# Optimization experiments

Hardware: AMD Instinct MI355X
Metric: run time of the kernel (lower is better)

The kernel has to match this reference:

```python
import jax, jax.numpy as jnp
import numpy as np

N = 50000
HEADS = 3
NEG_SLOPE = 0.2


def _add_self_loops(edge_index, num_nodes):
    loops = jnp.arange(num_nodes, dtype=edge_index.dtype)
    return jnp.concatenate([edge_index, jnp.stack([loops, loops])], axis=1)


def _gcn_conv(x, edge_index, W, b):
    # PyG GCNConv: add self loops, symmetric deg^-1/2 normalization.
    ei = _add_self_loops(edge_index, x.shape[0])
    src, dst = ei[0], ei[1]
    deg = jax.ops.segment_sum(jnp.ones_like(dst, dtype=x.dtype), dst, num_segments=x.shape[0])
    dinv = jax.lax.rsqrt(deg)  # deg >= 1 due to self loops
    norm = dinv[src] * dinv[dst]                      # [E']
    xw = x @ W                                        # [N, F_out]
    out = jax.ops.segment_sum(xw[src] * norm[:, None], dst, num_segments=x.shape[0])
    return out + b


def _gat_conv(x, edge_index, W, att_src, att_dst, b):
    # PyG GATConv (concat=True): self loops, per-edge attention, segment softmax.
    n = x.shape[0]
    ei = _add_self_loops(edge_index, n)
    src, dst = ei[0], ei[1]
    h = (x @ W).reshape(n, HEADS, -1)                 # [N, H, C]
    a_s = (h * att_src).sum(-1)                       # [N, H]
    a_d = (h * att_dst).sum(-1)                       # [N, H]
    e = jax.nn.leaky_relu(a_s[src] + a_d[dst], NEG_SLOPE)   # [E', H]
    m = jax.ops.segment_max(e, dst, num_segments=n)   # [N, H] per-dst max
    e = jnp.exp(e - m[dst])
    s = jax.ops.segment_sum(e, dst, num_segments=n)   # [N, H]
    alpha = e / s[dst]                                # [E', H]
    out = jax.ops.segment_sum(h[src] * alpha[:, :, None], dst, num_segments=n)
    return out.reshape(n, -1) + b                     # [N, H*C]


def setup_inputs() -> dict:
    key = jax.random.key(0)
    ks = jax.random.split(key, 9)
    in_ch, out_ch = 256, 64
    hid = 2 * out_ch  # 128
    E = 800000
    x = jax.random.normal(ks[0], (N, in_ch), dtype=jnp.float32)
    edge_index = jax.random.randint(ks[1], (2, E), 0, N, dtype=jnp.int32)
    W1 = jax.random.normal(ks[2], (in_ch, hid), dtype=jnp.float32) / np.sqrt(in_ch)
    b1 = jnp.zeros((hid,), dtype=jnp.float32)
    W2 = jax.random.normal(ks[3], (hid, HEADS * out_ch), dtype=jnp.float32) / np.sqrt(hid)
    att_src = jax.random.normal(ks[4], (HEADS, out_ch), dtype=jnp.float32) / np.sqrt(out_ch)
    att_dst = jax.random.normal(ks[5], (HEADS, out_ch), dtype=jnp.float32) / np.sqrt(out_ch)
    b2 = jnp.zeros((HEADS * out_ch,), dtype=jnp.float32)
    return {"x": x, "edge_index": edge_index, "W1": W1, "b1": b1,
            "W2": W2, "att_src": att_src, "att_dst": att_dst, "b2": b2}


def reference(x, edge_index, W1, b1, W2, att_src, att_dst, b2):
    h = jax.nn.relu(_gcn_conv(x, edge_index, W1, b1))
    # F.dropout(training=False) is identity in eval mode
    h = _gat_conv(h, edge_index, W2, att_src, att_dst, b2)
    return jax.nn.relu(h)
```

## Files before the change

kernel.cpp:

```cpp
#include <hip/hip_runtime.h>
#include <hip/hip_fp16.h>
#include <math.h>

#define NODES    50000
#define IN_CH    256
#define HID      128
#define HEADS    3
#define HC       64
#define OC       (HEADS*HC)
#define NEG_SLOPE 0.2f

typedef _Float16 half8_t __attribute__((ext_vector_type(8)));
typedef _Float16 half4_t __attribute__((ext_vector_type(4)));
typedef float float4_t __attribute__((ext_vector_type(4)));

__device__ __forceinline__ float lrelu(float v) { return v > 0.f ? v : NEG_SLOPE * v; }

__device__ __forceinline__ unsigned fkey(float f) {
    unsigned b = __float_as_uint(f);
    return (b & 0x80000000u) ? ~b : (b | 0x80000000u);
}
__device__ __forceinline__ float fdec(unsigned k) {
    unsigned b = (k & 0x80000000u) ? (k ^ 0x80000000u) : ~k;
    return __uint_as_float(b);
}

__global__ __launch_bounds__(256) void k_hist(const int* __restrict__ dst, int E, int* __restrict__ cnt,
                                              unsigned short* __restrict__ rank,
                                              const float* __restrict__ W1, const float* __restrict__ W2,
                                              _Float16* __restrict__ W1t, _Float16* __restrict__ W2t) {
    int e = blockIdx.x * 256 + threadIdx.x;
    if (e < E) {
        int r = atomicAdd(&cnt[dst[e]], 1);
        rank[e] = (unsigned short)r;
    }
    if (e < IN_CH * HID) {
        int c = e >> 8, k = e & 255;
        W1t[e] = (_Float16)W1[(size_t)k * HID + c];
    } else if (e < IN_CH * HID + HID * OC) {
        int u = e - IN_CH * HID;
        int c = u >> 7, k = u & 127;
        W2t[u] = (_Float16)W2[(size_t)k * OC + c];
    }
}

__global__ __launch_bounds__(1024) void k_scanA(const int* __restrict__ cnt, int* __restrict__ off,
                                                float* __restrict__ dinv, int* __restrict__ bsum, int n) {
    __shared__ int wsums[16];
    int tid = threadIdx.x, lane = tid & 63, wid = tid >> 6;
    int i = blockIdx.x * 1024 + tid;
    int v = (i < n) ? cnt[i] : 0;
    int incl = v;
    #pragma unroll
    for (int d = 1; d < 64; d <<= 1) {
        int t = __shfl_up(incl, d, 64);
        if (lane >= d) incl += t;
    }
    if (lane == 63) wsums[wid] = incl;
    __syncthreads();
    if (tid == 0) {
        int run = 0;
        #pragma unroll
        for (int j = 0; j < 16; j++) { int t = wsums[j]; wsums[j] = run; run += t; }
        bsum[blockIdx.x] = run;
    }
    __syncthreads();
    if (i < n) {
        off[i] = wsums[wid] + incl - v;
        dinv[i] = rsqrtf((float)(v + 1));
    }
}

__global__ __launch_bounds__(64) void k_scanB(const int* __restrict__ bsum, int* __restrict__ bbase,
                                              int* __restrict__ off, int nb, int n) {
    int tid = threadIdx.x;
    int v = (tid < nb) ? bsum[tid] : 0;
    int incl = v;
    #pragma unroll
    for (int d = 1; d < 64; d <<= 1) {
        int t = __shfl_up(incl, d, 64);
        if (tid >= d) incl += t;
    }
    bbase[tid] = incl - v;
    if (tid == 63) off[n] = incl;
}

__global__ __launch_bounds__(256) void k_scanC(int* __restrict__ off, const int* __restrict__ bbase, int n) {
    int i = blockIdx.x * 256 + threadIdx.x;
    if (i < n) off[i] += bbase[i >> 10];
}

__global__ __launch_bounds__(256) void k_fillg1(const int* __restrict__ src, const int* __restrict__ dst, int E,
                                                const int* __restrict__ off, const unsigned short* __restrict__ rank,
                                                unsigned short* __restrict__ csr,
                                                const float* __restrict__ x, const _Float16* __restrict__ W1t,
                                                const float* __restrict__ dinv, _Float16* __restrict__ xwh,
                                                int n, int fillBlocks) {
    if ((int)blockIdx.x < fillBlocks) {
        int e = blockIdx.x * 256 + threadIdx.x;
        if (e < E) {
            int d = dst[e];
            int p = off[d] + (int)rank[e];
            csr[p] = (unsigned short)src[e];
        }
        return;
    }

    int bid = blockIdx.x - fillBlocks;
    int wid = threadIdx.x >> 6, lane = threadIdx.x & 63;
    int lrow = lane & 15, kgrp = lane >> 4;
    int arow = bid * 64 + wid * 16 + lrow;
    bool rv = arow < n;
    const float* xp = x + (size_t)arow * IN_CH + kgrp * 8;

    float4_t acc[8];
    #pragma unroll
    for (int s = 0; s < 8; s++) acc[s] = (float4_t)(0.f);

    #pragma unroll
    for (int kc = 0; kc < IN_CH; kc += 32) {
        float4 a0, a1;
        if (rv) { a0 = *(const float4*)(xp + kc); a1 = *(const float4*)(xp + kc + 4); }
        else { a0 = make_float4(0.f,0.f,0.f,0.f); a1 = a0; }
        half8_t af;
        af[0]=(_Float16)a0.x; af[1]=(_Float16)a0.y; af[2]=(_Float16)a0.z; af[3]=(_Float16)a0.w;
        af[4]=(_Float16)a1.x; af[5]=(_Float16)a1.y; af[6]=(_Float16)a1.z; af[7]=(_Float16)a1.w;
        #pragma unroll
        for (int s = 0; s < 8; s++) {
            const _Float16* bp = W1t + (size_t)(s * 16 + lrow) * IN_CH + kc + kgrp * 8;
            half8_t bf = *(const half8_t*)bp;
            acc[s] = __builtin_amdgcn_mfma_f32_16x16x32_f16(af, bf, acc[s], 0, 0, 0);
        }
    }

    int orow0 = bid * 64 + wid * 16 + kgrp * 4;
    #pragma unroll
    for (int r = 0; r < 4; r++) {
        int orow = orow0 + r;
        if (orow < n) {
            float sc = dinv[orow];
            _Float16* po = xwh + ((size_t)orow << 7) + lrow;
            #pragma unroll
            for (int s = 0; s < 8; s++) po[s * 16] = (_Float16)(sc * acc[s][r]);
        }
    }
}

__global__ __launch_bounds__(256) void k_gcn(const _Float16* __restrict__ xwh, const unsigned short* __restrict__ csr,
                                             const int* __restrict__ off, const float* __restrict__ dinv,
                                             const float* __restrict__ b1, _Float16* __restrict__ hh, int n) {
    int w = (blockIdx.x * 256 + threadIdx.x) >> 6;
    int lane = threadIdx.x & 63;
    if (w >= n) return;
    int egrp = lane >> 4;
    int c8 = (lane & 15) * 8;
    float acc[8];
    #pragma unroll
    for (int j = 0; j < 8; j++) acc[j] = 0.f;

    int beg = off[w], end = off[w + 1];
    int i = beg;
    for (; i + 16 <= end; i += 16) {
        int s0 = csr[i + egrp];
        int s1 = csr[i + 4 + egrp];
        int s2 = csr[i + 8 + egrp];
        int s3 = csr[i + 12 + egrp];
        half8_t v0 = *(const half8_t*)(xwh + ((size_t)s0 << 7) + c8);
        half8_t v1 = *(const half8_t*)(xwh + ((size_t)s1 << 7) + c8);
        half8_t v2 = *(const half8_t*)(xwh + ((size_t)s2 << 7) + c8);
        half8_t v3 = *(const half8_t*)(xwh + ((size_t)s3 << 7) + c8);
        half8_t p01 = v0 + v1;
        half8_t p23 = v2 + v3;
        #pragma unroll
        for (int j = 0; j < 8; j++)
            acc[j] += (float)p01[j] + (float)p23[j];
    }
    for (; i + 4 <= end; i += 4) {
        int s = csr[i + egrp];
        half8_t v = *(const half8_t*)(xwh + ((size_t)s << 7) + c8);
        #pragma unroll
        for (int j = 0; j < 8; j++) acc[j] += (float)v[j];
    }
    if (i < end && egrp < (end - i)) {
        int s = csr[i + egrp];
        half8_t v = *(const half8_t*)(xwh + ((size_t)s << 7) + c8);
        #pragma unroll
        for (int j = 0; j < 8; j++) acc[j] += (float)v[j];
    }

    #pragma unroll
    for (int j = 0; j < 8; j++) {
        acc[j] += __shfl_xor(acc[j], 16, 64);
        acc[j] += __shfl_xor(acc[j], 32, 64);
    }
    if (egrp == 0) {
        float di = dinv[w];
        half8_t self = *(const half8_t*)(xwh + ((size_t)w << 7) + c8);
        float4 bb0 = *(const float4*)(b1 + c8);
        float4 bb1 = *(const float4*)(b1 + c8 + 4);
        float bv[8] = {bb0.x, bb0.y, bb0.z, bb0.w, bb1.x, bb1.y, bb1.z, bb1.w};
        half8_t o;
        #pragma unroll
        for (int j = 0; j < 8; j++)
            o[j] = (_Float16)fmaxf(fmaf(di, acc[j] + (float)self[j], bv[j]), 0.f);
        *(half8_t*)(hh + ((size_t)w << 7) + c8) = o;
    }
}

__global__ __launch_bounds__(256) void k_gemm2m(const _Float16* __restrict__ hh, const _Float16* __restrict__ W2t,
                                                _Float16* __restrict__ h2h, int n) {
    int wid = threadIdx.x >> 6, lane = threadIdx.x & 63;
    int lrow = lane & 15, kgrp = lane >> 4;
    int arow = blockIdx.x * 64 + wid * 16 + lrow;
    bool rv = arow < n;
    const _Float16* hp = hh + ((size_t)arow << 7) + kgrp * 8;

    float4_t acc[12];
    #pragma unroll
    for (int s = 0; s < 12; s++) acc[s] = (float4_t)(0.f);

    #pragma unroll
    for (int kc = 0; kc < HID; kc += 32) {
        half8_t af = (half8_t)((_Float16)0.f);
        if (rv) af = *(const half8_t*)(hp + kc);
        #pragma unroll
        for (int s = 0; s < 12; s++) {
            const _Float16* bp = W2t + (size_t)(s * 16 + lrow) * HID + kc + kgrp * 8;
            half8_t bf = *(const half8_t*)bp;
            acc[s] = __builtin_amdgcn_mfma_f32_16x16x32_f16(af, bf, acc[s], 0, 0, 0);
        }
    }

    int orow0 = blockIdx.x * 64 + wid * 16 + kgrp * 4;
    #pragma unroll
    for (int r = 0; r < 4; r++) {
        int orow = orow0 + r;
        if (orow < n) {
            _Float16* po = h2h + ((size_t)orow << 8) + lrow;
            #pragma unroll
            for (int s = 0; s < 12; s++) po[s * 16] = (_Float16)acc[s][r];
        }
    }
}

__global__ __launch_bounds__(256) void k_att(const _Float16* __restrict__ h2h, const float* __restrict__ att_s,
                                             const float* __restrict__ att_d, float* __restrict__ a_s4,
                                             float* __restrict__ a_d4, int n) {
    int w = (blockIdx.x * 256 + threadIdx.x) >> 6;
    int lane = threadIdx.x & 63;
    if (w >= n) return;
    bool act = lane < 48;
    int ll = act ? lane : (lane - 48);
    int hd = ll >> 4;
    int c4 = ll * 4;

    half4_t hv = *(const half4_t*)(h2h + ((size_t)w << 8) + c4);
    float4 as = *(const float4*)(att_s + c4);
    float4 ad = *(const float4*)(att_d + c4);
    float vs = (float)hv[0] * as.x + (float)hv[1] * as.y + (float)hv[2] * as.z + (float)hv[3] * as.w;
    float vd = (float)hv[0] * ad.x + (float)hv[1] * ad.y + (float)hv[2] * ad.z + (float)hv[3] * ad.w;
    #pragma unroll
    for (int o = 1; o < 16; o <<= 1) {
        vs += __shfl_xor(vs, o, 64);
        vd += __shfl_xor(vd, o, 64);
    }
    if (act && (ll & 15) == 0) {
        a_s4[w * 4 + hd] = vs;
        a_d4[w * 4 + hd] = vd;
    }
}

__global__ __launch_bounds__(1024) void k_asmax(const float* __restrict__ a_s4, int n, unsigned* __restrict__ asmaxk) {
    int i = blockIdx.x * 1024 + threadIdx.x;
    float m0 = -1e30f, m1 = -1e30f, m2 = -1e30f;
    if (i < n) {
        float4 v = *(const float4*)(a_s4 + (size_t)i * 4);
        m0 = v.x; m1 = v.y; m2 = v.z;
    }
    #pragma unroll
    for (int o = 32; o > 0; o >>= 1) {
        m0 = fmaxf(m0, __shfl_xor(m0, o, 64));
        m1 = fmaxf(m1, __shfl_xor(m1, o, 64));
        m2 = fmaxf(m2, __shfl_xor(m2, o, 64));
    }
    __shared__ float sm[16][3];
    int lane = threadIdx.x & 63, wid = threadIdx.x >> 6;
    if (lane == 0) { sm[wid][0] = m0; sm[wid][1] = m1; sm[wid][2] = m2; }
    __syncthreads();
    if (threadIdx.x == 0) {
        for (int j = 1; j < 16; j++) {
            m0 = fmaxf(m0, sm[j][0]); m1 = fmaxf(m1, sm[j][1]); m2 = fmaxf(m2, sm[j][2]);
        }
        atomicMax(asmaxk + 0, fkey(m0));
        atomicMax(asmaxk + 1, fkey(m1));
        atomicMax(asmaxk + 2, fkey(m2));
    }
}

#define GAT_EDGE(ev, hv) do { \
    float wl = __expf(lrelu((ev) + adh) - Ch); \
    ssum += wl; \
    a0 = fmaf(wl, (float)(hv)[0], a0); \
    a1 = fmaf(wl, (float)(hv)[1], a1); \
    a2 = fmaf(wl, (float)(hv)[2], a2); \
    a3 = fmaf(wl, (float)(hv)[3], a3); \
} while (0)

__global__ __launch_bounds__(256) void k_gat(const _Float16* __restrict__ h2h, const unsigned short* __restrict__ csr,
                                             const int* __restrict__ off, const float* __restrict__ a_s4,
                                             const float* __restrict__ a_d4, const unsigned* __restrict__ asmaxk,
                                             const float* __restrict__ b2, float* __restrict__ out, int n) {
    int w = (blockIdx.x * 256 + threadIdx.x) >> 6;
    int lane = threadIdx.x & 63;
    if (w >= n) return;
    bool act = lane < 48;
    int ll = act ? lane : (lane - 48);
    int hd = ll >> 4;
    int c4 = ll * 4;

    float adh = a_d4[w * 4 + hd];
    float Ch  = lrelu(fdec(asmaxk[hd]) + adh);
    float ash = a_s4[w * 4 + hd];
    float wsl = __expf(lrelu(ash + adh) - Ch);
    float ssum = wsl;
    half4_t hv = *(const half4_t*)(h2h + ((size_t)w << 8) + c4);
    float a0 = wsl * (float)hv[0], a1 = wsl * (float)hv[1];
    float a2 = wsl * (float)hv[2], a3 = wsl * (float)hv[3];

    int beg = off[w], end = off[w + 1];
    int i = beg;
    for (; i + 4 <= end; i += 4) {
        int sA = csr[i], sB = csr[i + 1], sC = csr[i + 2], sD = csr[i + 3];
        float eA = a_s4[(size_t)sA * 4 + hd];
        float eB = a_s4[(size_t)sB * 4 + hd];
        float eC = a_s4[(size_t)sC * 4 + hd];
        float eD = a_s4[(size_t)sD * 4 + hd];
        half4_t hA = *(const half4_t*)(h2h + ((size_t)sA << 8) + c4);
        half4_t hB = *(const half4_t*)(h2h + ((size_t)sB << 8) + c4);
        half4_t hC = *(const half4_t*)(h2h + ((size_t)sC << 8) + c4);
        half4_t hD = *(const half4_t*)(h2h + ((size_t)sD << 8) + c4);
        GAT_EDGE(eA, hA); GAT_EDGE(eB, hB); GAT_EDGE(eC, hC); GAT_EDGE(eD, hD);
    }
    for (; i < end; i++) {
        int s = csr[i];
        float ev = a_s4[(size_t)s * 4 + hd];
        half4_t hx = *(const half4_t*)(h2h + ((size_t)s << 8) + c4);
        GAT_EDGE(ev, hx);
    }

    if (act) {
        float inv = 1.f / ssum;
        float4 bb = *(const float4*)(b2 + c4);
        float4 o;
        o.x = fmaxf(fmaf(a0, inv, bb.x), 0.f);
        o.y = fmaxf(fmaf(a1, inv, bb.y), 0.f);
        o.z = fmaxf(fmaf(a2, inv, bb.z), 0.f);
        o.w = fmaxf(fmaf(a3, inv, bb.w), 0.f);
        *(float4*)(out + (size_t)w * OC + c4) = o;
    }
}

extern "C" void kernel_launch(void* const* d_in, const int* in_sizes, int n_in,
                              void* d_out, int out_size, void* d_ws, size_t ws_size,
                              hipStream_t stream) {
    const float* x        = (const float*)d_in[0];
    const int*   ei       = (const int*)d_in[1];
    const float* W1       = (const float*)d_in[2];
    const float* b1       = (const float*)d_in[3];
    const float* W2       = (const float*)d_in[4];
    const float* att_src  = (const float*)d_in[5];
    const float* att_dst  = (const float*)d_in[6];
    const float* b2       = (const float*)d_in[7];
    float* out = (float*)d_out;

    const int n = in_sizes[0] / IN_CH;
    const int E = in_sizes[1] / 2;
    const int* src = ei;
    const int* dst = ei + E;

    char* ws = (char*)d_ws;
    int*            cnt    = (int*)(ws + 0);
    unsigned*       asmaxk = (unsigned*)(ws + 200704);
    int*            off    = (int*)(ws + 200960);
    float*          dinv   = (float*)(ws + 401664);
    int*            bsum   = (int*)(ws + 602368);
    int*            bbase  = (int*)(ws + 602624);
    _Float16*       W1t    = (_Float16*)(ws + 602880);
    _Float16*       W2t    = (_Float16*)(ws + 668416);
    unsigned short* csr    = (unsigned short*)(ws + 717568);
    unsigned short* rank   = (unsigned short*)(ws + 2317568);
    float*          a_s4   = (float*)(ws + 3917568);
    float*          a_d4   = (float*)(ws + 4717568);
    _Float16*       xwh    = (_Float16*)(ws + 5517568);
    _Float16*       hh     = (_Float16*)(ws + 18317568);
    _Float16*       h2h    = (_Float16*)(ws + 31117568);

    (void)hipMemsetAsync(ws, 0, 200720, stream);

    int egrid = (E + 255) / 256;
    int nb = (n + 1023) / 1024;
    int gm = (n + 63) / 64;
    k_hist<<<egrid, 256, 0, stream>>>(dst, E, cnt, rank, W1, W2, W1t, W2t);
    k_scanA<<<nb, 1024, 0, stream>>>(cnt, off, dinv, bsum, n);
    k_scanB<<<1, 64, 0, stream>>>(bsum, bbase, off, nb, n);
    k_scanC<<<(n + 255) / 256, 256, 0, stream>>>(off, bbase, n);

    k_fillg1<<<egrid + gm, 256, 0, stream>>>(src, dst, E, off, rank, csr,
                                             x, W1t, dinv, xwh, n, egrid);

    int ngrid = (n + 3) / 4;
    k_gcn<<<ngrid, 256, 0, stream>>>(xwh, csr, off, dinv, b1, hh, n);

    k_gemm2m<<<gm, 256, 0, stream>>>(hh, W2t, h2h, n);

    k_att<<<ngrid, 256, 0, stream>>>(h2h, att_src, att_dst, a_s4, a_d4, n);
    k_asmax<<<nb, 1024, 0, stream>>>(a_s4, n, asmaxk);
    k_gat<<<ngrid, 256, 0, stream>>>(h2h, csr, off, a_s4, a_d4, asmaxk, b2, out, n);
}
```

Baseline: 224.3 us.

## Fuse attention-score computation into second GEMM and compact h2 row stride

Merges the separate attention-coefficient kernel into the second GEMM: each block stages its output tile in shared memory and computes per-head a_s/a_d dot products from there, so h2 is not re-read from global memory and one launch is removed. The h2 row stride also shrinks from 256 to 192 halves, which cuts the buffer footprint and makes the gathers in the GAT kernel denser. The cost is extra shared memory, a block barrier, and a serial 16-row loop per wave in the GEMM kernel.

```diff
diff --git a/kernel.cpp b/kernel.cpp
--- a/kernel.cpp
+++ b/kernel.cpp
@@ -207,8 +207,11 @@
     }
 }
 
-__global__ __launch_bounds__(256) void k_gemm2m(const _Float16* __restrict__ hh, const _Float16* __restrict__ W2t,
-                                                _Float16* __restrict__ h2h, int n) {
+__global__ __launch_bounds__(256) void k_gemm2att(const _Float16* __restrict__ hh, const _Float16* __restrict__ W2t,
+                                                  const float* __restrict__ att_s, const float* __restrict__ att_d,
+                                                  _Float16* __restrict__ h2h, float* __restrict__ a_s4,
+                                                  float* __restrict__ a_d4, int n) {
+    __shared__ _Float16 hs2[64][200];
     int wid = threadIdx.x >> 6, lane = threadIdx.x & 63;
     int lrow = lane & 15, kgrp = lane >> 4;
     int arow = blockIdx.x * 64 + wid * 16 + lrow;
@@ -235,38 +238,43 @@
     #pragma unroll
     for (int r = 0; r < 4; r++) {
         int orow = orow0 + r;
+        int rloc = wid * 16 + kgrp * 4 + r;
         if (orow < n) {
-            _Float16* po = h2h + ((size_t)orow << 8) + lrow;
+            _Float16* po = h2h + (size_t)orow * OC + lrow;
             #pragma unroll
-            for (int s = 0; s < 12; s++) po[s * 16] = (_Float16)acc[s][r];
-        }
-    }
-}
-
-__global__ __launch_bounds__(256) void k_att(const _Float16* __restrict__ h2h, const float* __restrict__ att_s,
-                                             const float* __restrict__ att_d, float* __restrict__ a_s4,
-                                             float* __restrict__ a_d4, int n) {
-    int w = (blockIdx.x * 256 + threadIdx.x) >> 6;
-    int lane = threadIdx.x & 63;
-    if (w >= n) return;
+            for (int s = 0; s < 12; s++) {
+                _Float16 hv = (_Float16)acc[s][r];
+                po[s * 16] = hv;
+                hs2[rloc][s * 16 + lrow] = hv;
+            }
+        } else {
+            #pragma unroll
+            for (int s = 0; s < 12; s++) hs2[rloc][s * 16 + lrow] = (_Float16)0.f;
+        }
+    }
+    __syncthreads();
+
     bool act = lane < 48;
     int ll = act ? lane : (lane - 48);
     int hd = ll >> 4;
     int c4 = ll * 4;
-
-    half4_t hv = *(const half4_t*)(h2h + ((size_t)w << 8) + c4);
     float4 as = *(const float4*)(att_s + c4);
     float4 ad = *(const float4*)(att_d + c4);
-    float vs = (float)hv[0] * as.x + (float)hv[1] * as.y + (float)hv[2] * as.z + (float)hv[3] * as.w;
-    float vd = (float)hv[0] * ad.x + (float)hv[1] * ad.y + (float)hv[2] * ad.z + (float)hv[3] * ad.w;
-    #pragma unroll
-    for (int o = 1; o < 16; o <<= 1) {
-        vs += __shfl_xor(vs, o, 64);
-        vd += __shfl_xor(vd, o, 64);
-    }
-    if (act && (ll & 15) == 0) {
-        a_s4[w * 4 + hd] = vs;
-        a_d4[w * 4 + hd] = vd;
+    for (int j = 0; j < 16; j++) {
+        int rloc = wid * 16 + j;
+        int orow = blockIdx.x * 64 + rloc;
+        half4_t hv = *(const half4_t*)&hs2[rloc][c4];
+        float vs = (float)hv[0] * as.x + (float)hv[1] * as.y + (float)hv[2] * as.z + (float)hv[3] * as.w;
+        float vd = (float)hv[0] * ad.x + (float)hv[1] * ad.y + (float)hv[2] * ad.z + (float)hv[3] * ad.w;
+        #pragma unroll
+        for (int o = 1; o < 16; o <<= 1) {
+            vs += __shfl_xor(vs, o, 64);
+            vd += __shfl_xor(vd, o, 64);
+        }
+        if (act && (ll & 15) == 0 && orow < n) {
+            a_s4[orow * 4 + hd] = vs;
+            a_d4[orow * 4 + hd] = vd;
+        }
     }
 }
 
@@ -323,7 +331,7 @@
     float ash = a_s4[w * 4 + hd];
     float wsl = __expf(lrelu(ash + adh) - Ch);
     float ssum = wsl;
-    half4_t hv = *(const half4_t*)(h2h + ((size_t)w << 8) + c4);
+    half4_t hv = *(const half4_t*)(h2h + (size_t)w * OC + c4);
     float a0 = wsl * (float)hv[0], a1 = wsl * (float)hv[1];
     float a2 = wsl * (float)hv[2], a3 = wsl * (float)hv[3];
 
@@ -335,16 +343,16 @@
         float eB = a_s4[(size_t)sB * 4 + hd];
         float eC = a_s4[(size_t)sC * 4 + hd];
         float eD = a_s4[(size_t)sD * 4 + hd];
-        half4_t hA = *(const half4_t*)(h2h + ((size_t)sA << 8) + c4);
-        half4_t hB = *(const half4_t*)(h2h + ((size_t)sB << 8) + c4);
-        half4_t hC = *(const half4_t*)(h2h + ((size_t)sC << 8) + c4);
-        half4_t hD = *(const half4_t*)(h2h + ((size_t)sD << 8) + c4);
+        half4_t hA = *(const half4_t*)(h2h + (size_t)sA * OC + c4);
+        half4_t hB = *(const half4_t*)(h2h + (size_t)sB * OC + c4);
+        half4_t hC = *(const half4_t*)(h2h + (size_t)sC * OC + c4);
+        half4_t hD = *(const half4_t*)(h2h + (size_t)sD * OC + c4);
         GAT_EDGE(eA, hA); GAT_EDGE(eB, hB); GAT_EDGE(eC, hC); GAT_EDGE(eD, hD);
     }
     for (; i < end; i++) {
         int s = csr[i];
         float ev = a_s4[(size_t)s * 4 + hd];
-        half4_t hx = *(const half4_t*)(h2h + ((size_t)s << 8) + c4);
+        half4_t hx = *(const half4_t*)(h2h + (size_t)s * OC + c4);
         GAT_EDGE(ev, hx);
     }
 
@@ -411,9 +419,8 @@
     int ngrid = (n + 3) / 4;
     k_gcn<<<ngrid, 256, 0, stream>>>(xwh, csr, off, dinv, b1, hh, n);
 
-    k_gemm2m<<<gm, 256, 0, stream>>>(hh, W2t, h2h, n);
-
-    k_att<<<ngrid, 256, 0, stream>>>(h2h, att_src, att_dst, a_s4, a_d4, n);
+    k_gemm2att<<<gm, 256, 0, stream>>>(hh, W2t, att_src, att_dst, h2h, a_s4, a_d4, n);
+
     k_asmax<<<nb, 1024, 0, stream>>>(a_s4, n, asmaxk);
     k_gat<<<ngrid, 256, 0, stream>>>(h2h, csr, off, a_s4, a_d4, asmaxk, b2, out, n);
 }
```

New measurement: 224.8 us. Within noise of the previous version (+0.2%).
